# Kernel tuning notes

Measured on AMD Instinct MI355X. Metric: run time of the kernel, lower is better.

The kernel has to match this reference:

```python
import jax, jax.numpy as jnp
import numpy as np

N = 50000      # atoms
E = 800000     # edges (flat neighbor list)
ELEM = 64      # elem_fea_len
NBR = 64       # nbr_fea_len
EPS = 1e-5


def _bn(x, gamma, beta):
    # BatchNorm1d in training mode: biased batch stats over dim 0
    mean = jnp.mean(x, axis=0)
    var = jnp.mean(jnp.square(x - mean), axis=0)
    return (x - mean) * jax.lax.rsqrt(var + EPS) * gamma + beta


def setup_inputs() -> dict:
    key = jax.random.key(0)
    ks = jax.random.split(key, 8)
    atom_in_fea = jax.random.normal(ks[0], (N, ELEM), dtype=jnp.float32)
    nbr_fea = jax.random.normal(ks[1], (E, NBR), dtype=jnp.float32)
    self_fea_idx = jnp.sort(jax.random.randint(ks[2], (E,), 0, N))
    nbr_fea_idx = jax.random.randint(ks[3], (E,), 0, N)
    d_in = 2 * ELEM + NBR
    d_out = 2 * ELEM
    W = jax.random.normal(ks[4], (d_in, d_out), dtype=jnp.float32) / np.sqrt(d_in)
    b = jax.random.normal(ks[5], (d_out,), dtype=jnp.float32) * 0.01
    bn1_gamma = jnp.ones((d_out,), jnp.float32)
    bn1_beta = jnp.zeros((d_out,), jnp.float32)
    bn2_gamma = jnp.ones((ELEM,), jnp.float32)
    bn2_beta = jnp.zeros((ELEM,), jnp.float32)
    return {
        "atom_in_fea": atom_in_fea, "nbr_fea": nbr_fea,
        "self_fea_idx": self_fea_idx, "nbr_fea_idx": nbr_fea_idx,
        "W": W, "b": b,
        "bn1_gamma": bn1_gamma, "bn1_beta": bn1_beta,
        "bn2_gamma": bn2_gamma, "bn2_beta": bn2_beta,
    }


def reference(atom_in_fea, nbr_fea, self_fea_idx, nbr_fea_idx,
              W, b, bn1_gamma, bn1_beta, bn2_gamma, bn2_beta):
    n_atoms = atom_in_fea.shape[0]
    # gather endpoint features: (E, ELEM) each
    atom_self = atom_in_fea[self_fea_idx]
    atom_nbr = atom_in_fea[nbr_fea_idx]
    total = jnp.concatenate([atom_self, atom_nbr, nbr_fea], axis=1)  # (E, 2*ELEM+NBR)
    total = total @ W + b                                            # (E, 2*ELEM)
    total = _bn(total, bn1_gamma, bn1_beta)
    filter_fea, core_fea = jnp.split(total, 2, axis=1)
    nbr_msg = jax.nn.sigmoid(filter_fea) * jax.nn.softplus(core_fea)  # (E, ELEM)
    nbr_sumed = jax.ops.segment_sum(nbr_msg, self_fea_idx, num_segments=n_atoms)
    nbr_sumed = _bn(nbr_sumed, bn2_gamma, bn2_beta)
    return jax.nn.softplus(atom_in_fea + nbr_sumed)
```

## Files before the change

### kernel.cpp

```cpp
#include <hip/hip_runtime.h>

typedef unsigned short ushort_t;
typedef __attribute__((ext_vector_type(8))) short short8;
typedef __attribute__((ext_vector_type(4))) float f32x4;

constexpr int N_ATOMS = 50000;
constexpr int N_EDGES = 800000;
constexpr int ELEM    = 64;
constexpr int D_IN    = 192;
constexpr int D_OUT   = 128;
constexpr float EPS   = 1e-5f;

constexpr int NREP   = 16;

constexpr int EDGE_TILE       = 64;
constexpr int TILES_PER_BLOCK = 5;
constexpr int GEMM_BLOCKS     = N_EDGES / (EDGE_TILE * TILES_PER_BLOCK);
static_assert(N_EDGES % (EDGE_TILE * TILES_PER_BLOCK) == 0, "even split");

constexpr size_t OFF_NS   = 0;
constexpr size_t OFF_ABF  = OFF_NS   + (size_t)N_ATOMS * ELEM * 4;
constexpr size_t OFF_WT   = OFF_ABF  + (size_t)N_ATOMS * ELEM * 2;
constexpr size_t OFF_BN1  = OFF_WT   + (size_t)D_OUT * D_IN * 2;
constexpr size_t OFF_SC1  = OFF_BN1  + NREP * 256 * 4;
constexpr size_t OFF_BN2  = OFF_SC1  + 256 * 4;
constexpr size_t OFF_SC2  = OFF_BN2  + NREP * 128 * 4;

__device__ __forceinline__ ushort_t f32_to_bf16(float f) {
    unsigned int u = __float_as_uint(f);
    u = (u + 0x7fffu + ((u >> 16) & 1u)) >> 16;
    return (ushort_t)u;
}
__device__ __forceinline__ float softplus_f(float x) {
    return fmaxf(x, 0.f) + __logf(1.f + __expf(-fabsf(x)));
}
__device__ __forceinline__ short8 pack8(float4 a, float4 b) {
    short8 r;
    r[0] = (short)f32_to_bf16(a.x); r[1] = (short)f32_to_bf16(a.y);
    r[2] = (short)f32_to_bf16(a.z); r[3] = (short)f32_to_bf16(a.w);
    r[4] = (short)f32_to_bf16(b.x); r[5] = (short)f32_to_bf16(b.y);
    r[6] = (short)f32_to_bf16(b.z); r[7] = (short)f32_to_bf16(b.w);
    return r;
}

__global__ void prep_init_kernel(const float* __restrict__ atom, const float* __restrict__ W,
                                 ushort_t* __restrict__ abf, ushort_t* __restrict__ Wt,
                                 float* __restrict__ ns,
                                 float* __restrict__ bn1r, float* __restrict__ bn2r) {
    int i = blockIdx.x * blockDim.x + threadIdx.x;
    if (i < N_ATOMS * ELEM) { abf[i] = f32_to_bf16(atom[i]); ns[i] = 0.f; }
    if (i < D_IN * D_OUT) {
        int k = i >> 7, n = i & 127;
        Wt[n * D_IN + k] = f32_to_bf16(W[i]);
    }
    if (i < NREP * 256) bn1r[i] = 0.f;
    if (i < NREP * 128) bn2r[i] = 0.f;
}

constexpr int BS_USHORTS = 4 * 6 * 64 * 8;

__device__ __forceinline__ void stage_tile(ushort_t* __restrict__ Bs,
                                           const ushort_t* __restrict__ abf,
                                           const float* __restrict__ nbrf,
                                           const int* __restrict__ sidx,
                                           const int* __restrict__ nidx,
                                           int e0, int tid) {
    #pragma unroll
    for (int half = 0; half < 2; ++half) {
        int c = tid + half * 256;
        int e = c >> 3, h = c & 7;
        int gg = e >> 4, m16 = e & 15;
        int kss = h >> 2, quad = h & 3;
        int rs = sidx[e0 + e];
        int rn = nidx[e0 + e];
        uint4 vs = *(const uint4*)(abf + (size_t)rs * 64 + h * 8);
        uint4 vn = *(const uint4*)(abf + (size_t)rn * 64 + h * 8);
        const float* pf = nbrf + (size_t)(e0 + e) * 64 + h * 8;
        float4 fa = *(const float4*)pf;
        float4 fb = *(const float4*)(pf + 4);
        *(uint4*)&Bs[((gg * 6 + 0 + kss) * 64 + m16 * 4 + quad) * 8] = vs;
        *(uint4*)&Bs[((gg * 6 + 2 + kss) * 64 + m16 * 4 + quad) * 8] = vn;
        short8 pk = pack8(fa, fb);
        *(short8*)&Bs[((gg * 6 + 4 + kss) * 64 + m16 * 4 + quad) * 8] = pk;
    }
}

__global__ __launch_bounds__(256) void stats_kernel(
    const ushort_t* __restrict__ abf, const float* __restrict__ nbrf,
    const int* __restrict__ sidx, const int* __restrict__ nidx,
    const ushort_t* __restrict__ Wt, float* __restrict__ bn1r)
{
    __shared__ __align__(16) ushort_t Bs[BS_USHORTS];
    const int tid  = threadIdx.x;
    const int wave = tid >> 6, lane = tid & 63;
    const int m16  = lane & 15, quad = lane >> 4;

    short8 wfrag[2][6];
    #pragma unroll
    for (int t = 0; t < 2; ++t) {
        const ushort_t* wp = Wt + (size_t)(t * 64 + wave * 16 + m16) * D_IN + quad * 8;
        #pragma unroll
        for (int ks = 0; ks < 6; ++ks) wfrag[t][ks] = *(const short8*)(wp + ks * 32);
    }

    float s[2][4] = {{0.f,0.f,0.f,0.f},{0.f,0.f,0.f,0.f}};
    float q[2][4] = {{0.f,0.f,0.f,0.f},{0.f,0.f,0.f,0.f}};

    for (int t = 0; t < TILES_PER_BLOCK; ++t) {
        const int e0 = (blockIdx.x * TILES_PER_BLOCK + t) * EDGE_TILE;
        stage_tile(Bs, abf, nbrf, sidx, nidx, e0, tid);
        __syncthreads();

        #pragma unroll
        for (int gg = 0; gg < 4; ++gg) {
            short8 bf[6];
            #pragma unroll
            for (int ks = 0; ks < 6; ++ks)
                bf[ks] = *(const short8*)&Bs[((gg * 6 + ks) * 64 + m16 * 4 + quad) * 8];

            f32x4 acc0 = {0.f,0.f,0.f,0.f}, acc1 = {0.f,0.f,0.f,0.f};
            #pragma unroll
            for (int ks = 0; ks < 6; ++ks) {
                acc0 = __builtin_amdgcn_mfma_f32_16x16x32_bf16(wfrag[0][ks], bf[ks], acc0, 0, 0, 0);
                acc1 = __builtin_amdgcn_mfma_f32_16x16x32_bf16(wfrag[1][ks], bf[ks], acc1, 0, 0, 0);
            }
            #pragma unroll
            for (int r = 0; r < 4; ++r) {
                float v0 = acc0[r], v1 = acc1[r];
                s[0][r] += v0; q[0][r] += v0 * v0;
                s[1][r] += v1; q[1][r] += v1 * v1;
            }
        }
        __syncthreads();
    }

    float* rep = bn1r + (size_t)(blockIdx.x & (NREP - 1)) * 256;
    #pragma unroll
    for (int t = 0; t < 2; ++t)
        #pragma unroll
        for (int r = 0; r < 4; ++r) {
            float sv = s[t][r], qv = q[t][r];
            #pragma unroll
            for (int d = 1; d < 16; d <<= 1) {
                sv += __shfl_xor(sv, d);
                qv += __shfl_xor(qv, d);
            }
            if (m16 == 0) {
                int c = t * 64 + wave * 16 + quad * 4 + r;
                atomicAdd(&rep[c], sv);
                atomicAdd(&rep[128 + c], qv);
            }
        }
}

__global__ void bn1_finalize(const float* __restrict__ bn1r,
                             const float* __restrict__ g1, const float* __restrict__ b1,
                             float* __restrict__ sc) {
    int c = threadIdx.x;
    float s = 0.f, q = 0.f;
    #pragma unroll
    for (int r = 0; r < NREP; ++r) { s += bn1r[r * 256 + c]; q += bn1r[r * 256 + 128 + c]; }
    float mean = s * (1.f / N_EDGES);
    float var  = q * (1.f / N_EDGES) - mean * mean;
    float scale = g1[c] * rsqrtf(var + EPS);
    sc[c] = scale;
    sc[128 + c] = b1[c] - mean * scale;
}

__global__ __launch_bounds__(256) void msg_kernel(
    const ushort_t* __restrict__ abf, const float* __restrict__ nbrf,
    const int* __restrict__ sidx, const int* __restrict__ nidx,
    const ushort_t* __restrict__ Wt, const float* __restrict__ sc,
    float* __restrict__ ns)
{
    __shared__ __align__(16) ushort_t Bs[BS_USHORTS];
    __shared__ int ss[EDGE_TILE];
    const int tid  = threadIdx.x;
    const int wave = tid >> 6, lane = tid & 63;
    const int m16  = lane & 15, quad = lane >> 4;

    short8 wfrag[2][6];
    #pragma unroll
    for (int t = 0; t < 2; ++t) {
        const ushort_t* wp = Wt + (size_t)(t * 64 + wave * 16 + m16) * D_IN + quad * 8;
        #pragma unroll
        for (int ks = 0; ks < 6; ++ks) wfrag[t][ks] = *(const short8*)(wp + ks * 32);
    }

    float scf[4], shf[4], scc[4], shc[4];
    #pragma unroll
    for (int r = 0; r < 4; ++r) {
        int cf = wave * 16 + quad * 4 + r;
        scf[r] = sc[cf];       shf[r] = sc[128 + cf];
        scc[r] = sc[64 + cf];  shc[r] = sc[192 + cf];
    }

    for (int t = 0; t < TILES_PER_BLOCK; ++t) {
        const int e0 = (blockIdx.x * TILES_PER_BLOCK + t) * EDGE_TILE;
        stage_tile(Bs, abf, nbrf, sidx, nidx, e0, tid);
        if (tid < EDGE_TILE) ss[tid] = sidx[e0 + tid];
        __syncthreads();

        #pragma unroll
        for (int gg = 0; gg < 4; ++gg) {
            short8 bf[6];
            #pragma unroll
            for (int ks = 0; ks < 6; ++ks)
                bf[ks] = *(const short8*)&Bs[((gg * 6 + ks) * 64 + m16 * 4 + quad) * 8];

            f32x4 acc0 = {0.f,0.f,0.f,0.f}, acc1 = {0.f,0.f,0.f,0.f};
            #pragma unroll
            for (int ks = 0; ks < 6; ++ks) {
                acc0 = __builtin_amdgcn_mfma_f32_16x16x32_bf16(wfrag[0][ks], bf[ks], acc0, 0, 0, 0);
                acc1 = __builtin_amdgcn_mfma_f32_16x16x32_bf16(wfrag[1][ks], bf[ks], acc1, 0, 0, 0);
            }

            float m[4];
            #pragma unroll
            for (int r = 0; r < 4; ++r) {
                float yf = fmaf(acc0[r], scf[r], shf[r]);
                float yc = fmaf(acc1[r], scc[r], shc[r]);
                m[r] = softplus_f(yc) / (1.f + __expf(-yf));
            }

            int a = ss[gg * 16 + m16];
            #pragma unroll
            for (int d = 1; d < 16; d <<= 1) {
                int   au = __shfl_up(a,    d, 16);
                float u0 = __shfl_up(m[0], d, 16);
                float u1 = __shfl_up(m[1], d, 16);
                float u2 = __shfl_up(m[2], d, 16);
                float u3 = __shfl_up(m[3], d, 16);
                if (m16 >= d && au == a) { m[0] += u0; m[1] += u1; m[2] += u2; m[3] += u3; }
            }
            int an = __shfl_down(a, 1, 16);
            if (m16 == 15 || an != a) {
                float* p = ns + (size_t)a * 64 + wave * 16 + quad * 4;
                atomicAdd(p + 0, m[0]); atomicAdd(p + 1, m[1]);
                atomicAdd(p + 2, m[2]); atomicAdd(p + 3, m[3]);
            }
        }
        __syncthreads();
    }
}

__global__ __launch_bounds__(256) void bn2_stats_kernel(
    const float* __restrict__ ns, float* __restrict__ bn2r)
{
    int c = threadIdx.x & 63;
    float s = 0.f, q = 0.f;
    for (int a = blockIdx.x * 4 + (threadIdx.x >> 6); a < N_ATOMS; a += 4096) {
        float v = ns[a * ELEM + c];
        s += v; q += v * v;
    }
    float* rep = bn2r + (size_t)(blockIdx.x & (NREP - 1)) * 128;
    atomicAdd(&rep[c], s);
    atomicAdd(&rep[64 + c], q);
}

__global__ void bn2_finalize(const float* __restrict__ bn2r,
                             const float* __restrict__ g2, const float* __restrict__ b2,
                             float* __restrict__ sc2) {
    int c = threadIdx.x;
    float s = 0.f, q = 0.f;
    #pragma unroll
    for (int r = 0; r < NREP; ++r) { s += bn2r[r * 128 + c]; q += bn2r[r * 128 + 64 + c]; }
    float mean = s * (1.f / N_ATOMS);
    float var  = q * (1.f / N_ATOMS) - mean * mean;
    float scale = g2[c] * rsqrtf(var + EPS);
    sc2[c] = scale;
    sc2[64 + c] = b2[c] - mean * scale;
}

__global__ void final_kernel(const float* __restrict__ atom, const float* __restrict__ ns,
                             const float* __restrict__ sc2, float* __restrict__ out)
{
    int i = blockIdx.x * blockDim.x + threadIdx.x;
    if (i < N_ATOMS * ELEM) {
        int c = i & 63;
        float x = atom[i] + fmaf(ns[i], sc2[c], sc2[64 + c]);
        out[i] = softplus_f(x);
    }
}

extern "C" void kernel_launch(void* const* d_in, const int* in_sizes, int n_in,
                              void* d_out, int out_size, void* d_ws, size_t ws_size,
                              hipStream_t stream) {
    const float* atom = (const float*)d_in[0];
    const float* nbrf = (const float*)d_in[1];
    const int*   sidx = (const int*)d_in[2];
    const int*   nidx = (const int*)d_in[3];
    const float* W    = (const float*)d_in[4];
    const float* g1   = (const float*)d_in[6];
    const float* b1   = (const float*)d_in[7];
    const float* g2   = (const float*)d_in[8];
    const float* b2   = (const float*)d_in[9];
    float* out = (float*)d_out;
    char*  ws  = (char*)d_ws;

    float*    ns   = (float*)(ws + OFF_NS);
    ushort_t* abf  = (ushort_t*)(ws + OFF_ABF);
    ushort_t* Wt   = (ushort_t*)(ws + OFF_WT);
    float*    bn1r = (float*)(ws + OFF_BN1);
    float*    sc1  = (float*)(ws + OFF_SC1);
    float*    bn2r = (float*)(ws + OFF_BN2);
    float*    sc2  = (float*)(ws + OFF_SC2);

    hipLaunchKernelGGL(prep_init_kernel, dim3((N_ATOMS * ELEM + 255) / 256), dim3(256), 0, stream,
                       atom, W, abf, Wt, ns, bn1r, bn2r);
    hipLaunchKernelGGL(stats_kernel, dim3(GEMM_BLOCKS), dim3(256), 0, stream,
                       abf, nbrf, sidx, nidx, Wt, bn1r);
    hipLaunchKernelGGL(bn1_finalize, dim3(1), dim3(128), 0, stream, bn1r, g1, b1, sc1);
    hipLaunchKernelGGL(msg_kernel, dim3(GEMM_BLOCKS), dim3(256), 0, stream,
                       abf, nbrf, sidx, nidx, Wt, sc1, ns);
    hipLaunchKernelGGL(bn2_stats_kernel, dim3(1024), dim3(256), 0, stream, ns, bn2r);
    hipLaunchKernelGGL(bn2_finalize, dim3(1), dim3(64), 0, stream, bn2r, g2, b2, sc2);
    hipLaunchKernelGGL(final_kernel, dim3((N_ATOMS * ELEM + 255) / 256), dim3(256), 0, stream,
                       atom, ns, sc2, out);
}
```

Baseline: 486.3 us.

## Double-buffer edge tile staging with register prefetch in stats and msg kernels

Splits tile staging into a global-load phase into registers and a later LDS write phase. The next tile's gathers are issued before the current tile's MFMA work, with two LDS buffers so one barrier per tile suffices. The edge-to-thread mapping is also rearranged so each lane's staging slot matches its MFMA read slot (lane-linear addressing), and bf16 packing now uses the paired conversion intrinsic. This costs roughly double the LDS and extra registers held across the compute loop, which may reduce occupancy.

```diff
diff --git a/kernel.cpp b/kernel.cpp
--- a/kernel.cpp
+++ b/kernel.cpp
@@ -1,4 +1,5 @@
 #include <hip/hip_runtime.h>
+#include <hip/hip_bf16.h>
 
 typedef unsigned short ushort_t;
 typedef __attribute__((ext_vector_type(8))) short short8;
@@ -34,13 +35,15 @@
 __device__ __forceinline__ float softplus_f(float x) {
     return fmaxf(x, 0.f) + __logf(1.f + __expf(-fabsf(x)));
 }
+__device__ __forceinline__ unsigned pkbits(float lo, float hi) {
+    __hip_bfloat162 h = __float22bfloat162_rn(make_float2(lo, hi));
+    union { __hip_bfloat162 h2; unsigned u; } cv; cv.h2 = h; return cv.u;
+}
 __device__ __forceinline__ short8 pack8(float4 a, float4 b) {
-    short8 r;
-    r[0] = (short)f32_to_bf16(a.x); r[1] = (short)f32_to_bf16(a.y);
-    r[2] = (short)f32_to_bf16(a.z); r[3] = (short)f32_to_bf16(a.w);
-    r[4] = (short)f32_to_bf16(b.x); r[5] = (short)f32_to_bf16(b.y);
-    r[6] = (short)f32_to_bf16(b.z); r[7] = (short)f32_to_bf16(b.w);
-    return r;
+    union { uint4 u4; short8 s8; } cv;
+    cv.u4.x = pkbits(a.x, a.y); cv.u4.y = pkbits(a.z, a.w);
+    cv.u4.z = pkbits(b.x, b.y); cv.u4.w = pkbits(b.z, b.w);
+    return cv.s8;
 }
 
 __global__ void prep_init_kernel(const float* __restrict__ atom, const float* __restrict__ W,
@@ -59,29 +62,41 @@
 
 constexpr int BS_USHORTS = 4 * 6 * 64 * 8;
 
-__device__ __forceinline__ void stage_tile(ushort_t* __restrict__ Bs,
+struct StageRegs {
+    int   rs;
+    uint4 vs[2], vn[2];
+    float4 fa[2], fb[2];
+};
+
+__device__ __forceinline__ void stage_load(StageRegs& R,
                                            const ushort_t* __restrict__ abf,
                                            const float* __restrict__ nbrf,
                                            const int* __restrict__ sidx,
                                            const int* __restrict__ nidx,
                                            int e0, int tid) {
-    #pragma unroll
-    for (int half = 0; half < 2; ++half) {
-        int c = tid + half * 256;
-        int e = c >> 3, h = c & 7;
-        int gg = e >> 4, m16 = e & 15;
-        int kss = h >> 2, quad = h & 3;
-        int rs = sidx[e0 + e];
-        int rn = nidx[e0 + e];
-        uint4 vs = *(const uint4*)(abf + (size_t)rs * 64 + h * 8);
-        uint4 vn = *(const uint4*)(abf + (size_t)rn * 64 + h * 8);
-        const float* pf = nbrf + (size_t)(e0 + e) * 64 + h * 8;
-        float4 fa = *(const float4*)pf;
-        float4 fb = *(const float4*)(pf + 4);
-        *(uint4*)&Bs[((gg * 6 + 0 + kss) * 64 + m16 * 4 + quad) * 8] = vs;
-        *(uint4*)&Bs[((gg * 6 + 2 + kss) * 64 + m16 * 4 + quad) * 8] = vn;
-        short8 pk = pack8(fa, fb);
-        *(short8*)&Bs[((gg * 6 + 4 + kss) * 64 + m16 * 4 + quad) * 8] = pk;
+    const int w = tid & 63, v = tid >> 6;
+    const int el = v * 16 + (w & 15);
+    const int rs = sidx[e0 + el], rn = nidx[e0 + el];
+    R.rs = rs;
+    #pragma unroll
+    for (int hf = 0; hf < 2; ++hf) {
+        int h = (w >> 4) + hf * 4;
+        R.vs[hf] = *(const uint4*)(abf + (size_t)rs * 64 + h * 8);
+        R.vn[hf] = *(const uint4*)(abf + (size_t)rn * 64 + h * 8);
+        const float* pf = nbrf + (size_t)(e0 + el) * 64 + h * 8;
+        R.fa[hf] = *(const float4*)pf;
+        R.fb[hf] = *(const float4*)(pf + 4);
+    }
+}
+
+__device__ __forceinline__ void stage_write(ushort_t* __restrict__ Bs,
+                                            const StageRegs& R, int tid) {
+    const int w = tid & 63, v = tid >> 6;
+    #pragma unroll
+    for (int hf = 0; hf < 2; ++hf) {
+        *(uint4*)&Bs[((v * 6 + 0 + hf) * 64 + w) * 8] = R.vs[hf];
+        *(uint4*)&Bs[((v * 6 + 2 + hf) * 64 + w) * 8] = R.vn[hf];
+        *(short8*)&Bs[((v * 6 + 4 + hf) * 64 + w) * 8] = pack8(R.fa[hf], R.fb[hf]);
     }
 }
 
@@ -90,10 +105,11 @@
     const int* __restrict__ sidx, const int* __restrict__ nidx,
     const ushort_t* __restrict__ Wt, float* __restrict__ bn1r)
 {
-    __shared__ __align__(16) ushort_t Bs[BS_USHORTS];
+    __shared__ __align__(16) ushort_t Bs[2][BS_USHORTS];
     const int tid  = threadIdx.x;
     const int wave = tid >> 6, lane = tid & 63;
     const int m16  = lane & 15, quad = lane >> 4;
+    const int base = blockIdx.x * TILES_PER_BLOCK * EDGE_TILE;
 
     short8 wfrag[2][6];
     #pragma unroll
@@ -106,17 +122,22 @@
     float s[2][4] = {{0.f,0.f,0.f,0.f},{0.f,0.f,0.f,0.f}};
     float q[2][4] = {{0.f,0.f,0.f,0.f},{0.f,0.f,0.f,0.f}};
 
+    StageRegs R;
+    stage_load(R, abf, nbrf, sidx, nidx, base, tid);
+    stage_write(Bs[0], R, tid);
+    __syncthreads();
+
     for (int t = 0; t < TILES_PER_BLOCK; ++t) {
-        const int e0 = (blockIdx.x * TILES_PER_BLOCK + t) * EDGE_TILE;
-        stage_tile(Bs, abf, nbrf, sidx, nidx, e0, tid);
-        __syncthreads();
+        const int cur = t & 1;
+        if (t + 1 < TILES_PER_BLOCK)
+            stage_load(R, abf, nbrf, sidx, nidx, base + (t + 1) * EDGE_TILE, tid);
 
         #pragma unroll
         for (int gg = 0; gg < 4; ++gg) {
             short8 bf[6];
             #pragma unroll
             for (int ks = 0; ks < 6; ++ks)
-                bf[ks] = *(const short8*)&Bs[((gg * 6 + ks) * 64 + m16 * 4 + quad) * 8];
+                bf[ks] = *(const short8*)&Bs[cur][((gg * 6 + ks) * 64 + lane) * 8];
 
             f32x4 acc0 = {0.f,0.f,0.f,0.f}, acc1 = {0.f,0.f,0.f,0.f};
             #pragma unroll
@@ -131,6 +152,8 @@
                 s[1][r] += v1; q[1][r] += v1 * v1;
             }
         }
+
+        if (t + 1 < TILES_PER_BLOCK) stage_write(Bs[cur ^ 1], R, tid);
         __syncthreads();
     }
 
@@ -173,11 +196,12 @@
     const ushort_t* __restrict__ Wt, const float* __restrict__ sc,
     float* __restrict__ ns)
 {
-    __shared__ __align__(16) ushort_t Bs[BS_USHORTS];
-    __shared__ int ss[EDGE_TILE];
+    __shared__ __align__(16) ushort_t Bs[2][BS_USHORTS];
+    __shared__ int ss[2][EDGE_TILE];
     const int tid  = threadIdx.x;
     const int wave = tid >> 6, lane = tid & 63;
     const int m16  = lane & 15, quad = lane >> 4;
+    const int base = blockIdx.x * TILES_PER_BLOCK * EDGE_TILE;
 
     short8 wfrag[2][6];
     #pragma unroll
@@ -195,18 +219,23 @@
         scc[r] = sc[64 + cf];  shc[r] = sc[192 + cf];
     }
 
+    StageRegs R;
+    stage_load(R, abf, nbrf, sidx, nidx, base, tid);
+    stage_write(Bs[0], R, tid);
+    if (quad == 0) ss[0][wave * 16 + m16] = R.rs;
+    __syncthreads();
+
     for (int t = 0; t < TILES_PER_BLOCK; ++t) {
-        const int e0 = (blockIdx.x * TILES_PER_BLOCK + t) * EDGE_TILE;
-        stage_tile(Bs, abf, nbrf, sidx, nidx, e0, tid);
-        if (tid < EDGE_TILE) ss[tid] = sidx[e0 + tid];
-        __syncthreads();
+        const int cur = t & 1;
+        if (t + 1 < TILES_PER_BLOCK)
+            stage_load(R, abf, nbrf, sidx, nidx, base + (t + 1) * EDGE_TILE, tid);
 
         #pragma unroll
         for (int gg = 0; gg < 4; ++gg) {
             short8 bf[6];
             #pragma unroll
             for (int ks = 0; ks < 6; ++ks)
-                bf[ks] = *(const short8*)&Bs[((gg * 6 + ks) * 64 + m16 * 4 + quad) * 8];
+                bf[ks] = *(const short8*)&Bs[cur][((gg * 6 + ks) * 64 + lane) * 8];
 
             f32x4 acc0 = {0.f,0.f,0.f,0.f}, acc1 = {0.f,0.f,0.f,0.f};
             #pragma unroll
@@ -223,7 +252,7 @@
                 m[r] = softplus_f(yc) / (1.f + __expf(-yf));
             }
 
-            int a = ss[gg * 16 + m16];
+            int a = ss[cur][gg * 16 + m16];
             #pragma unroll
             for (int d = 1; d < 16; d <<= 1) {
                 int   au = __shfl_up(a,    d, 16);
@@ -239,6 +268,11 @@
                 atomicAdd(p + 0, m[0]); atomicAdd(p + 1, m[1]);
                 atomicAdd(p + 2, m[2]); atomicAdd(p + 3, m[3]);
             }
+        }
+
+        if (t + 1 < TILES_PER_BLOCK) {
+            stage_write(Bs[cur ^ 1], R, tid);
+            if (quad == 0) ss[cur ^ 1][wave * 16 + m16] = R.rs;
         }
         __syncthreads();
     }
```

Measured after the change: 508.7 us. 4.6% more time.
